# Kernel tuning notes

Hardware: AMD Instinct MI355X
Metric: run time of the kernel (lower is better)

## Reference

```python
import jax, jax.numpy as jnp
import numpy as np

N = 50000   # nodes
E = 800000  # edges (avg degree 16)
C = 96      # in = hidden = out channels


def setup_inputs() -> dict:
    key = jax.random.key(0)
    ks = jax.random.split(key, 8)
    s = np.float32(1.0 / np.sqrt(C))
    x = jax.random.normal(ks[0], (N, C), dtype=jnp.float32)
    edge_index = jax.random.randint(ks[1], (2, E), 0, N, dtype=jnp.int64)
    W1 = jax.random.normal(ks[2], (C, C), dtype=jnp.float32) * s
    Wr1 = jax.random.normal(ks[3], (C, C), dtype=jnp.float32) * s
    b1 = jnp.zeros((C,), dtype=jnp.float32)
    W2 = jax.random.normal(ks[4], (C, C), dtype=jnp.float32) * s
    Wr2 = jax.random.normal(ks[5], (C, C), dtype=jnp.float32) * s
    b2 = jnp.zeros((C,), dtype=jnp.float32)
    return {"x": x, "edge_index": edge_index,
            "W1": W1, "Wr1": Wr1, "b1": b1,
            "W2": W2, "Wr2": Wr2, "b2": b2}


def spline_conv(x, edge_index, W, W_root, b):
    """Gather-transform-scatter message passing (SplineConv core, mean aggr)."""
    src, dst = edge_index[0], edge_index[1]
    h = x @ W                                   # [N, C] transform once per node
    msg = h[src]                                # [E, C] edge gather
    agg = jax.ops.segment_sum(msg, dst, num_segments=N)        # scatter-add
    deg = jax.ops.segment_sum(jnp.ones((E,), x.dtype), dst, num_segments=N)
    agg = agg / jnp.maximum(deg, 1.0)[:, None]  # mean aggregation
    return agg + x @ W_root + b                 # root weight + bias


def reference(x, edge_index, W1, Wr1, b1, W2, Wr2, b2):
    h = jax.nn.relu(spline_conv(x, edge_index, W1, Wr1, b1))
    out = spline_conv(h, edge_index, W2, Wr2, b2)
    return out.reshape(-1)  # generalization of x.view(1600)
```

## Files before the change

### kernel.cpp

```cpp
#include <hip/hip_runtime.h>

#define C 96
#define BKT_SHIFT 9
#define BKT_SIZE 512
#define CAP 10240
#define EB 2048
typedef unsigned char u8;
typedef unsigned short u16;
typedef unsigned int u32;
typedef __attribute__((ext_vector_type(8))) short short8;
typedef __attribute__((ext_vector_type(4))) float floatx4;
typedef __attribute__((ext_vector_type(2))) float floatx2;

__device__ inline u16 f2bf(float f) {
    union { float f; u32 u; } v; v.f = f;
    u32 r = v.u + 0x7fff + ((v.u >> 16) & 1);
    return (u16)(r >> 16);
}
__device__ inline u32 pk4_fp8(float a, float b, float c, float d) {
    u32 w = 0;
    w = __builtin_amdgcn_cvt_pk_fp8_f32(a, b, w, false);
    w = __builtin_amdgcn_cvt_pk_fp8_f32(c, d, w, true);
    return w;
}
__device__ inline u8 f2fp8(float a) {
    return (u8)(__builtin_amdgcn_cvt_pk_fp8_f32(a, a, 0, false) & 0xff);
}

__global__ __launch_bounds__(256) void binA_kernel(const int* __restrict__ src,
                                                   const int* __restrict__ dst,
                                                   int* __restrict__ blk_cnt,
                                                   int* __restrict__ blk_off,
                                                   u32* __restrict__ stage, int E, int DB,
                                                   const float* __restrict__ x,
                                                   u16* __restrict__ xb,
                                                   u8* __restrict__ xf8, int n16, int CX,
                                                   const float* W0, const float* W1,
                                                   const float* W2, const float* W3,
                                                   u16* T0, u16* T1, u16* T2, u16* T3) {
    int bid = blockIdx.x;
    int t = threadIdx.x;
    if (bid >= DB) {
        if (bid < DB + CX) {
            int i = (bid - DB) * 256 + t;
            if (i >= n16) return;
            const float4* p = (const float4*)x + (size_t)i * 4;
            float4 a = p[0], b = p[1], c = p[2], d = p[3];
            short8 o0, o1;
            o0[0] = (short)f2bf(a.x); o0[1] = (short)f2bf(a.y);
            o0[2] = (short)f2bf(a.z); o0[3] = (short)f2bf(a.w);
            o0[4] = (short)f2bf(b.x); o0[5] = (short)f2bf(b.y);
            o0[6] = (short)f2bf(b.z); o0[7] = (short)f2bf(b.w);
            o1[0] = (short)f2bf(c.x); o1[1] = (short)f2bf(c.y);
            o1[2] = (short)f2bf(c.z); o1[3] = (short)f2bf(c.w);
            o1[4] = (short)f2bf(d.x); o1[5] = (short)f2bf(d.y);
            o1[6] = (short)f2bf(d.z); o1[7] = (short)f2bf(d.w);
            *(short8*)(xb + (size_t)i * 16) = o0;
            *(short8*)(xb + (size_t)i * 16 + 8) = o1;
            uint4 f8;
            f8.x = pk4_fp8(a.x, a.y, a.z, a.w);
            f8.y = pk4_fp8(b.x, b.y, b.z, b.w);
            f8.z = pk4_fp8(c.x, c.y, c.z, c.w);
            f8.w = pk4_fp8(d.x, d.y, d.z, d.w);
            *(uint4*)(xf8 + (size_t)i * 16) = f8;
        } else {
            int w = bid - DB - CX;
            const float* W = w == 0 ? W0 : w == 1 ? W1 : w == 2 ? W2 : W3;
            u16* T = w == 0 ? T0 : w == 1 ? T1 : w == 2 ? T2 : T3;
            for (int i = t; i < C * C; i += 256) {
                int k = i / C, n = i - k * C;
                T[n * C + k] = f2bf(W[i]);
            }
        }
        return;
    }

    __shared__ u32 s_word[EB];
    __shared__ int s_cnt[128];
    __shared__ int s_inc[128];
    int e0 = bid * EB;
    int cnt_here = min(EB, E - e0);

    for (int i = t; i < 128; i += 256) s_cnt[i] = 0;
    __syncthreads();

    int my_src[EB / 256], my_dl[EB / 256], my_b[EB / 256], my_rank[EB / 256];
    int nmine = 0;
#pragma unroll
    for (int k = 0; k < EB / 256; k++) {
        int i = t + k * 256;
        if (i < cnt_here) {
            int s = src[e0 + i], d = dst[e0 + i];
            int b = d >> BKT_SHIFT;
            my_src[nmine] = s;
            my_dl[nmine] = d & (BKT_SIZE - 1);
            my_b[nmine] = b;
            my_rank[nmine] = atomicAdd(&s_cnt[b], 1);
            nmine++;
        }
    }
    __syncthreads();

    if (t < 128) s_inc[t] = s_cnt[t];
    __syncthreads();
    for (int off = 1; off < 128; off <<= 1) {
        int x2 = (t >= off && t < 128) ? s_inc[t - off] : 0;
        __syncthreads();
        if (t < 128) s_inc[t] += x2;
        __syncthreads();
    }
    if (t < 128) {
        blk_cnt[bid * 128 + t] = s_cnt[t];
        blk_off[bid * 128 + t] = s_inc[t] - s_cnt[t];
    }

    for (int k = 0; k < nmine; k++) {
        int b = my_b[k];
        int slot = (s_inc[b] - s_cnt[b]) + my_rank[k];
        s_word[slot] = ((u32)my_dl[k] << 16) | (u32)my_src[k];
    }
    __syncthreads();

    for (int i = t; i < cnt_here; i += 256) stage[(size_t)bid * EB + i] = s_word[i];
}

__global__ __launch_bounds__(256) void binB_kernel(const u32* __restrict__ stage,
                                                   const int* __restrict__ blk_cnt,
                                                   const int* __restrict__ blk_off,
                                                   int* __restrict__ deg,
                                                   int* __restrict__ row_off,
                                                   u16* __restrict__ csr, int N, int DB) {
    __shared__ int cnt[BKT_SIZE];
    __shared__ int cur[BKT_SIZE];
    __shared__ int ssum[256];
    int b = blockIdx.x;
    int n0 = b << BKT_SHIFT;
    int nn = min(BKT_SIZE, N - n0);
    int t = threadIdx.x;
    int s0 = b * CAP;

    for (int i = t; i < BKT_SIZE; i += 256) cnt[i] = 0;
    __syncthreads();

    for (int i = t; i < DB; i += 256) {
        int len = blk_cnt[i * 128 + b];
        const u32* run = stage + (size_t)i * EB + blk_off[i * 128 + b];
        for (int j = 0; j < len; j++) atomicAdd(&cnt[run[j] >> 16], 1);
    }
    __syncthreads();

    int a0 = cnt[2 * t], a1 = cnt[2 * t + 1];
    ssum[t] = a0 + a1;
    __syncthreads();
    for (int off = 1; off < 256; off <<= 1) {
        int x = (t >= off) ? ssum[t - off] : 0;
        __syncthreads();
        ssum[t] += x;
        __syncthreads();
    }
    int excl = ssum[t] - (a0 + a1);
    if (2 * t < nn) { deg[n0 + 2 * t] = a0; row_off[n0 + 2 * t] = s0 + excl; }
    if (2 * t + 1 < nn) { deg[n0 + 2 * t + 1] = a1; row_off[n0 + 2 * t + 1] = s0 + excl + a0; }
    __syncthreads();
    cur[2 * t] = s0 + excl;
    cur[2 * t + 1] = s0 + excl + a0;
    __syncthreads();

    for (int i = t; i < DB; i += 256) {
        int len = blk_cnt[i * 128 + b];
        const u32* run = stage + (size_t)i * EB + blk_off[i * 128 + b];
        for (int j = 0; j < len; j++) {
            u32 w = run[j];
            int p = atomicAdd(&cur[w >> 16], 1);
            csr[p] = (u16)(w & 0xffffu);
        }
    }
}

template <bool RELU, bool WF8, typename OT>
__global__ __launch_bounds__(256, 4) void layer_kernel(const u16* __restrict__ Xbf,
                                                       const u8* __restrict__ Xf8,
                                                       const int* __restrict__ row_off,
                                                       const int* __restrict__ deg,
                                                       const u16* __restrict__ csr,
                                                       const u16* __restrict__ WTA,
                                                       const u16* __restrict__ WTR,
                                                       const float* __restrict__ BIAS,
                                                       OT* __restrict__ Y,
                                                       u8* __restrict__ Yf8, int n) {
    __shared__ u16 sA[64 * 104];
    __shared__ int s_dg[64];
    __shared__ int s_perm[64];
    const int t = threadIdx.x;
    const int row0 = blockIdx.x * 64;

    if (t < 64) {
        int node = row0 + t;
        s_dg[t] = (node < n) ? deg[node] : 0;
    }
    __syncthreads();
    if (t < 64) {
        int di = s_dg[t];
        int r = 0;
#pragma unroll 8
        for (int j = 0; j < 64; j++) {
            int dj = s_dg[j];
            r += (dj < di) || (dj == di && j < t);
        }
        s_perm[r] = t;
    }
    __syncthreads();

    {
        int nl = s_perm[t >> 2];
        int node = row0 + nl;
        int q = t & 3;
        float acc[24];
#pragma unroll
        for (int i = 0; i < 24; i++) acc[i] = 0.f;
        int d = 0;
        if (node < n) {
            int start = row_off[node];
            d = s_dg[nl];
            const u8* Xq = Xf8 + q * 24;
            int j = 0;
            for (; j + 4 <= d; j += 4) {
                int si[4];
#pragma unroll
                for (int k = 0; k < 4; k++) si[k] = csr[start + j + k];
                uint2 v[4][3];
#pragma unroll
                for (int k = 0; k < 4; k++) {
                    const u8* p = Xq + (size_t)si[k] * 96;
                    v[k][0] = *(const uint2*)(p);
                    v[k][1] = *(const uint2*)(p + 8);
                    v[k][2] = *(const uint2*)(p + 16);
                }
#pragma unroll
                for (int k = 0; k < 4; k++) {
                    u32 ws[6] = {v[k][0].x, v[k][0].y, v[k][1].x,
                                 v[k][1].y, v[k][2].x, v[k][2].y};
#pragma unroll
                    for (int i = 0; i < 6; i++) {
                        floatx2 lo = __builtin_amdgcn_cvt_pk_f32_fp8(ws[i], false);
                        floatx2 hi = __builtin_amdgcn_cvt_pk_f32_fp8(ws[i], true);
                        acc[4 * i]     += lo[0];
                        acc[4 * i + 1] += lo[1];
                        acc[4 * i + 2] += hi[0];
                        acc[4 * i + 3] += hi[1];
                    }
                }
            }
            for (; j < d; j++) {
                const u8* p = Xq + (size_t)csr[start + j] * 96;
                uint2 w0 = *(const uint2*)(p);
                uint2 w1 = *(const uint2*)(p + 8);
                uint2 w2 = *(const uint2*)(p + 16);
                u32 ws[6] = {w0.x, w0.y, w1.x, w1.y, w2.x, w2.y};
#pragma unroll
                for (int i = 0; i < 6; i++) {
                    floatx2 lo = __builtin_amdgcn_cvt_pk_f32_fp8(ws[i], false);
                    floatx2 hi = __builtin_amdgcn_cvt_pk_f32_fp8(ws[i], true);
                    acc[4 * i]     += lo[0];
                    acc[4 * i + 1] += lo[1];
                    acc[4 * i + 2] += hi[0];
                    acc[4 * i + 3] += hi[1];
                }
            }
        }
        float inv = 1.0f / fmaxf((float)d, 1.0f);
        u16* dl = sA + nl * 104 + q * 24;
#pragma unroll
        for (int c = 0; c < 3; c++) {
            short8 o;
#pragma unroll
            for (int i = 0; i < 8; i++) o[i] = (short)f2bf(acc[c * 8 + i] * inv);
            *(short8*)(dl + c * 8) = o;
        }
    }
    __syncthreads();

    const int lane = t & 63;
    const int w = t >> 6;
    const int quad = lane >> 4;
    const int l16 = lane & 15;
    const int r0 = row0 + w * 16;

    floatx4 acc6[6];
#pragma unroll
    for (int i = 0; i < 6; i++) acc6[i] = (floatx4){0.f, 0.f, 0.f, 0.f};

    {
        const u16* Ap = sA + (w * 16 + l16) * 104 + quad * 8;
        const u16* Wp = WTA + l16 * C + quad * 8;
#pragma unroll
        for (int ks = 0; ks < 3; ks++) {
            short8 a = *(const short8*)(Ap + ks * 32);
#pragma unroll
            for (int nt = 0; nt < 6; nt++) {
                short8 b = *(const short8*)(Wp + nt * 16 * C + ks * 32);
                acc6[nt] = __builtin_amdgcn_mfma_f32_16x16x32_bf16(a, b, acc6[nt], 0, 0, 0);
            }
        }
    }
    {
        int arow = r0 + l16;
        if (arow >= n) arow = n - 1;
        const u16* Xp = Xbf + (size_t)arow * C + quad * 8;
        const u16* Wp = WTR + l16 * C + quad * 8;
#pragma unroll
        for (int ks = 0; ks < 3; ks++) {
            short8 a = *(const short8*)(Xp + ks * 32);
#pragma unroll
            for (int nt = 0; nt < 6; nt++) {
                short8 b = *(const short8*)(Wp + nt * 16 * C + ks * 32);
                acc6[nt] = __builtin_amdgcn_mfma_f32_16x16x32_bf16(a, b, acc6[nt], 0, 0, 0);
            }
        }
    }

#pragma unroll
    for (int nt = 0; nt < 6; nt++) {
        int cc = nt * 16 + l16;
        float bv = BIAS[cc];
#pragma unroll
        for (int r = 0; r < 4; r++) {
            int row = r0 + quad * 4 + r;
            if (row >= n) continue;
            float v = acc6[nt][r] + bv;
            if (RELU) v = fmaxf(v, 0.f);
            if constexpr (sizeof(OT) == 2) Y[(size_t)row * C + cc] = (OT)f2bf(v);
            else                           Y[(size_t)row * C + cc] = (OT)v;
            if constexpr (WF8) Yf8[(size_t)row * 96 + cc] = f2fp8(v);
        }
    }
}

extern "C" void kernel_launch(void* const* d_in, const int* in_sizes, int n_in,
                              void* d_out, int out_size, void* d_ws, size_t ws_size,
                              hipStream_t stream) {
    const float* x   = (const float*)d_in[0];
    const int*   ei  = (const int*)d_in[1];
    const float* W1  = (const float*)d_in[2];
    const float* Wr1 = (const float*)d_in[3];
    const float* b1  = (const float*)d_in[4];
    const float* W2  = (const float*)d_in[5];
    const float* Wr2 = (const float*)d_in[6];
    const float* b2  = (const float*)d_in[7];
    float* out = (float*)d_out;

    const int N = in_sizes[0] / C;
    const int E = in_sizes[1] / 2;
    const int* src = ei;
    const int* dst = ei + E;

    const int nbkt = (N + BKT_SIZE - 1) >> BKT_SHIFT;
    const int DB   = (E + EB - 1) / EB;
    const int n16  = N * C / 16;
    const int CX   = (n16 + 255) / 256;
    int Npad = (N + 63) & ~63;

    int*  blk_cnt = (int*)d_ws;
    int*  blk_off = blk_cnt + DB * 128;
    int*  deg     = blk_off + DB * 128;
    int*  row_off = deg + Npad;
    u32*  stage   = (u32*)(row_off + Npad);
    u16*  csr     = (u16*)(stage + (size_t)DB * EB);
    u16*  xb      = csr + (((size_t)nbkt * CAP + 7) & ~(size_t)7);
    u16*  h1b     = xb + (size_t)N * C;
    u16*  wt      = h1b + (size_t)N * C;
    u16 *wt1 = wt, *wtr1 = wt + C * C, *wt2 = wt + 2 * C * C, *wtr2 = wt + 3 * C * C;
    u8*   xf8     = (u8*)(wt + 4 * C * C);
    u8*   h1f8    = xf8 + (size_t)N * 96;

    const int grid64 = (N + 63) / 64;

    binA_kernel<<<DB + CX + 4, 256, 0, stream>>>(src, dst, blk_cnt, blk_off, stage, E, DB,
                                                 x, xb, xf8, n16, CX,
                                                 W1, Wr1, W2, Wr2, wt1, wtr1, wt2, wtr2);
    binB_kernel<<<nbkt, 256, 0, stream>>>(stage, blk_cnt, blk_off, deg, row_off, csr, N, DB);

    layer_kernel<true, true, u16><<<grid64, 256, 0, stream>>>(
        xb, xf8, row_off, deg, csr, wt1, wtr1, b1, h1b, h1f8, N);
    layer_kernel<false, false, float><<<grid64, 256, 0, stream>>>(
        h1b, h1f8, row_off, deg, csr, wt2, wtr2, b2, out, h1f8, N);
}
```

Baseline: 174.2 us.

## Halve rows per block and split each node's edge gather across two threads

Each block now handles 32 nodes instead of 64. Eight threads per node split the edge list by parity and combine their partial sums with a shuffle-xor. The MFMA stage is reorganised so four waves cover a 2x2 grid of 16-row by 48-column tiles, and the launch bound is raised to 6 blocks per CU. The aim is more gather parallelism and memory-level parallelism per node, and better hiding of load latency. In exchange it adds the shuffle reduction, doubles the number of blocks and reloads weights per block, and may raise register pressure under the tighter occupancy bound.

```diff
diff --git a/kernel.cpp b/kernel.cpp
--- a/kernel.cpp
+++ b/kernel.cpp
@@ -178,7 +178,7 @@
 }
 
 template <bool RELU, bool WF8, typename OT>
-__global__ __launch_bounds__(256, 4) void layer_kernel(const u16* __restrict__ Xbf,
+__global__ __launch_bounds__(256, 6) void layer_kernel(const u16* __restrict__ Xbf,
                                                        const u8* __restrict__ Xf8,
                                                        const int* __restrict__ row_off,
                                                        const int* __restrict__ deg,
@@ -188,22 +188,22 @@
                                                        const float* __restrict__ BIAS,
                                                        OT* __restrict__ Y,
                                                        u8* __restrict__ Yf8, int n) {
-    __shared__ u16 sA[64 * 104];
-    __shared__ int s_dg[64];
-    __shared__ int s_perm[64];
+    __shared__ u16 sA[32 * 104];
+    __shared__ int s_dg[32];
+    __shared__ int s_perm[32];
     const int t = threadIdx.x;
-    const int row0 = blockIdx.x * 64;
-
-    if (t < 64) {
+    const int row0 = blockIdx.x * 32;
+
+    if (t < 32) {
         int node = row0 + t;
         s_dg[t] = (node < n) ? deg[node] : 0;
     }
     __syncthreads();
-    if (t < 64) {
+    if (t < 32) {
         int di = s_dg[t];
         int r = 0;
 #pragma unroll 8
-        for (int j = 0; j < 64; j++) {
+        for (int j = 0; j < 32; j++) {
             int dj = s_dg[j];
             r += (dj < di) || (dj == di && j < t);
         }
@@ -212,51 +212,35 @@
     __syncthreads();
 
     {
-        int nl = s_perm[t >> 2];
+        int nl = s_perm[t >> 3];
         int node = row0 + nl;
         int q = t & 3;
+        int h = (t >> 2) & 1;
+        int d = 0, start = 0;
+        if (node < n) { start = row_off[node]; d = s_dg[nl]; }
+
         float acc[24];
 #pragma unroll
         for (int i = 0; i < 24; i++) acc[i] = 0.f;
-        int d = 0;
-        if (node < n) {
-            int start = row_off[node];
-            d = s_dg[nl];
-            const u8* Xq = Xf8 + q * 24;
-            int j = 0;
-            for (; j + 4 <= d; j += 4) {
-                int si[4];
-#pragma unroll
-                for (int k = 0; k < 4; k++) si[k] = csr[start + j + k];
-                uint2 v[4][3];
-#pragma unroll
-                for (int k = 0; k < 4; k++) {
-                    const u8* p = Xq + (size_t)si[k] * 96;
-                    v[k][0] = *(const uint2*)(p);
-                    v[k][1] = *(const uint2*)(p + 8);
-                    v[k][2] = *(const uint2*)(p + 16);
-                }
-#pragma unroll
-                for (int k = 0; k < 4; k++) {
-                    u32 ws[6] = {v[k][0].x, v[k][0].y, v[k][1].x,
-                                 v[k][1].y, v[k][2].x, v[k][2].y};
-#pragma unroll
-                    for (int i = 0; i < 6; i++) {
-                        floatx2 lo = __builtin_amdgcn_cvt_pk_f32_fp8(ws[i], false);
-                        floatx2 hi = __builtin_amdgcn_cvt_pk_f32_fp8(ws[i], true);
-                        acc[4 * i]     += lo[0];
-                        acc[4 * i + 1] += lo[1];
-                        acc[4 * i + 2] += hi[0];
-                        acc[4 * i + 3] += hi[1];
-                    }
-                }
-            }
-            for (; j < d; j++) {
-                const u8* p = Xq + (size_t)csr[start + j] * 96;
-                uint2 w0 = *(const uint2*)(p);
-                uint2 w1 = *(const uint2*)(p + 8);
-                uint2 w2 = *(const uint2*)(p + 16);
-                u32 ws[6] = {w0.x, w0.y, w1.x, w1.y, w2.x, w2.y};
+        const u8* Xq = Xf8 + q * 24;
+
+        int j = h;
+        for (; j + 6 < d; j += 8) {
+            int si[4];
+#pragma unroll
+            for (int k = 0; k < 4; k++) si[k] = csr[start + j + 2 * k];
+            uint2 v[4][3];
+#pragma unroll
+            for (int k = 0; k < 4; k++) {
+                const u8* p = Xq + (size_t)si[k] * 96;
+                v[k][0] = *(const uint2*)(p);
+                v[k][1] = *(const uint2*)(p + 8);
+                v[k][2] = *(const uint2*)(p + 16);
+            }
+#pragma unroll
+            for (int k = 0; k < 4; k++) {
+                u32 ws[6] = {v[k][0].x, v[k][0].y, v[k][1].x,
+                             v[k][1].y, v[k][2].x, v[k][2].y};
 #pragma unroll
                 for (int i = 0; i < 6; i++) {
                     floatx2 lo = __builtin_amdgcn_cvt_pk_f32_fp8(ws[i], false);
@@ -268,14 +252,36 @@
                 }
             }
         }
-        float inv = 1.0f / fmaxf((float)d, 1.0f);
-        u16* dl = sA + nl * 104 + q * 24;
-#pragma unroll
-        for (int c = 0; c < 3; c++) {
-            short8 o;
-#pragma unroll
-            for (int i = 0; i < 8; i++) o[i] = (short)f2bf(acc[c * 8 + i] * inv);
-            *(short8*)(dl + c * 8) = o;
+        for (; j < d; j += 2) {
+            const u8* p = Xq + (size_t)csr[start + j] * 96;
+            uint2 w0 = *(const uint2*)(p);
+            uint2 w1 = *(const uint2*)(p + 8);
+            uint2 w2 = *(const uint2*)(p + 16);
+            u32 ws[6] = {w0.x, w0.y, w1.x, w1.y, w2.x, w2.y};
+#pragma unroll
+            for (int i = 0; i < 6; i++) {
+                floatx2 lo = __builtin_amdgcn_cvt_pk_f32_fp8(ws[i], false);
+                floatx2 hi = __builtin_amdgcn_cvt_pk_f32_fp8(ws[i], true);
+                acc[4 * i]     += lo[0];
+                acc[4 * i + 1] += lo[1];
+                acc[4 * i + 2] += hi[0];
+                acc[4 * i + 3] += hi[1];
+            }
+        }
+
+#pragma unroll
+        for (int i = 0; i < 24; i++) acc[i] += __shfl_xor(acc[i], 4);
+
+        if (h == 0) {
+            float inv = 1.0f / fmaxf((float)d, 1.0f);
+            u16* dl = sA + nl * 104 + q * 24;
+#pragma unroll
+            for (int c = 0; c < 3; c++) {
+                short8 o;
+#pragma unroll
+                for (int i = 0; i < 8; i++) o[i] = (short)f2bf(acc[c * 8 + i] * inv);
+                *(short8*)(dl + c * 8) = o;
+            }
         }
     }
     __syncthreads();
@@ -284,50 +290,51 @@
     const int w = t >> 6;
     const int quad = lane >> 4;
     const int l16 = lane & 15;
-    const int r0 = row0 + w * 16;
-
-    floatx4 acc6[6];
-#pragma unroll
-    for (int i = 0; i < 6; i++) acc6[i] = (floatx4){0.f, 0.f, 0.f, 0.f};
+    const int rw = (w & 1) * 16;
+    const int c0 = (w >> 1) * 48;
+
+    floatx4 acc3[3];
+#pragma unroll
+    for (int i = 0; i < 3; i++) acc3[i] = (floatx4){0.f, 0.f, 0.f, 0.f};
 
     {
-        const u16* Ap = sA + (w * 16 + l16) * 104 + quad * 8;
-        const u16* Wp = WTA + l16 * C + quad * 8;
+        const u16* Ap = sA + (rw + l16) * 104 + quad * 8;
+        const u16* Wp = WTA + (c0 + l16) * C + quad * 8;
 #pragma unroll
         for (int ks = 0; ks < 3; ks++) {
             short8 a = *(const short8*)(Ap + ks * 32);
 #pragma unroll
-            for (int nt = 0; nt < 6; nt++) {
+            for (int nt = 0; nt < 3; nt++) {
                 short8 b = *(const short8*)(Wp + nt * 16 * C + ks * 32);
-                acc6[nt] = __builtin_amdgcn_mfma_f32_16x16x32_bf16(a, b, acc6[nt], 0, 0, 0);
+                acc3[nt] = __builtin_amdgcn_mfma_f32_16x16x32_bf16(a, b, acc3[nt], 0, 0, 0);
             }
         }
     }
     {
-        int arow = r0 + l16;
+        int arow = row0 + rw + l16;
         if (arow >= n) arow = n - 1;
         const u16* Xp = Xbf + (size_t)arow * C + quad * 8;
-        const u16* Wp = WTR + l16 * C + quad * 8;
+        const u16* Wp = WTR + (c0 + l16) * C + quad * 8;
 #pragma unroll
         for (int ks = 0; ks < 3; ks++) {
             short8 a = *(const short8*)(Xp + ks * 32);
 #pragma unroll
-            for (int nt = 0; nt < 6; nt++) {
+            for (int nt = 0; nt < 3; nt++) {
                 short8 b = *(const short8*)(Wp + nt * 16 * C + ks * 32);
-                acc6[nt] = __builtin_amdgcn_mfma_f32_16x16x32_bf16(a, b, acc6[nt], 0, 0, 0);
-            }
-        }
-    }
-
-#pragma unroll
-    for (int nt = 0; nt < 6; nt++) {
-        int cc = nt * 16 + l16;
+                acc3[nt] = __builtin_amdgcn_mfma_f32_16x16x32_bf16(a, b, acc3[nt], 0, 0, 0);
+            }
+        }
+    }
+
+#pragma unroll
+    for (int nt = 0; nt < 3; nt++) {
+        int cc = c0 + nt * 16 + l16;
         float bv = BIAS[cc];
 #pragma unroll
         for (int r = 0; r < 4; r++) {
-            int row = r0 + quad * 4 + r;
+            int row = row0 + rw + quad * 4 + r;
             if (row >= n) continue;
-            float v = acc6[nt][r] + bv;
+            float v = acc3[nt][r] + bv;
             if (RELU) v = fmaxf(v, 0.f);
             if constexpr (sizeof(OT) == 2) Y[(size_t)row * C + cc] = (OT)f2bf(v);
             else                           Y[(size_t)row * C + cc] = (OT)v;
@@ -373,15 +380,15 @@
     u8*   xf8     = (u8*)(wt + 4 * C * C);
     u8*   h1f8    = xf8 + (size_t)N * 96;
 
-    const int grid64 = (N + 63) / 64;
+    const int grid32 = (N + 31) / 32;
 
     binA_kernel<<<DB + CX + 4, 256, 0, stream>>>(src, dst, blk_cnt, blk_off, stage, E, DB,
                                                  x, xb, xf8, n16, CX,
                                                  W1, Wr1, W2, Wr2, wt1, wtr1, wt2, wtr2);
     binB_kernel<<<nbkt, 256, 0, stream>>>(stage, blk_cnt, blk_off, deg, row_off, csr, N, DB);
 
-    layer_kernel<true, true, u16><<<grid64, 256, 0, stream>>>(
+    layer_kernel<true, true, u16><<<grid32, 256, 0, stream>>>(
         xb, xf8, row_off, deg, csr, wt1, wtr1, b1, h1b, h1f8, N);
-    layer_kernel<false, false, float><<<grid64, 256, 0, stream>>>(
+    layer_kernel<false, false, float><<<grid32, 256, 0, stream>>>(
         h1b, h1f8, row_off, deg, csr, wt2, wtr2, b2, out, h1f8, N);
 }
```

Result: slower. 206.8 us (+18.7%).
